# Kernel tuning notes

Measured on AMD Instinct MI355X. Metric: run time of the kernel, lower is better.

Reference implementation:

```python
import jax, jax.numpy as jnp
import numpy as np

N = 50000          # nodes
E = 800000         # edges (before self-loops)
F_IN = 256         # feature_dim
HEADS = 3
OUT = 128          # per-head channels
HO = HEADS * OUT   # 384
NUM_GRAPHS = 64
NUM_CLASSES = 2
SLOPE = 0.2        # PyG GATConv default negative_slope


def setup_inputs() -> dict:
    key = jax.random.key(0)
    ks = jax.random.split(key, 8)
    x = jax.random.normal(ks[0], (N, F_IN), dtype=jnp.float32)
    edge_index = jax.random.randint(ks[1], (2, E), 0, N)
    batch = jnp.sort(jax.random.randint(ks[2], (N,), 0, NUM_GRAPHS))
    # GATConv params (glorot-ish scales)
    W = jax.random.normal(ks[3], (F_IN, HO), dtype=jnp.float32) * (1.0 / np.sqrt(F_IN))
    att_src = jax.random.normal(ks[4], (HEADS, OUT), dtype=jnp.float32) * 0.1
    att_dst = jax.random.normal(ks[5], (HEADS, OUT), dtype=jnp.float32) * 0.1
    bias = jnp.zeros((HO,), dtype=jnp.float32)
    fc_w = jax.random.normal(ks[6], (HO, NUM_CLASSES), dtype=jnp.float32) * 0.05
    fc_b = jnp.zeros((NUM_CLASSES,), dtype=jnp.float32)
    return {"x": x, "edge_index": edge_index, "batch": batch, "W": W,
            "att_src": att_src, "att_dst": att_dst, "bias": bias,
            "fc_w": fc_w, "fc_b": fc_b}


def reference(x, edge_index, batch, W, att_src, att_dst, bias, fc_w, fc_b):
    n = x.shape[0]
    h = (x @ W).reshape(n, HEADS, OUT)                      # [N, H, C]
    # add self-loops (PyG default add_self_loops=True)
    loops = jnp.arange(n)
    src = jnp.concatenate([edge_index[0], loops])           # [E+N]
    dst = jnp.concatenate([edge_index[1], loops])
    # per-node attention logits
    a_src = jnp.einsum('nhc,hc->nh', h, att_src)            # [N, H]
    a_dst = jnp.einsum('nhc,hc->nh', h, att_dst)
    e = jax.nn.leaky_relu(a_src[src] + a_dst[dst], SLOPE)   # [E+N, H]
    # segment softmax over incoming edges of each dst node
    emax = jax.ops.segment_max(e, dst, num_segments=n)
    ex = jnp.exp(e - emax[dst])
    denom = jax.ops.segment_sum(ex, dst, num_segments=n)
    alpha = ex / (denom[dst] + 1e-16)                       # [E+N, H]
    # weighted scatter-add aggregation
    msg = h[src] * alpha[:, :, None]                        # [E+N, H, C]
    out = jax.ops.segment_sum(msg, dst, num_segments=n)     # [N, H, C]
    out = jax.nn.relu(out.reshape(n, HO) + bias)            # [N, 384]
    # global mean pool per graph
    counts = jax.ops.segment_sum(jnp.ones((n,), out.dtype), batch,
                                 num_segments=NUM_GRAPHS)
    pooled = jax.ops.segment_sum(out, batch, num_segments=NUM_GRAPHS)
    pooled = pooled / jnp.maximum(counts, 1.0)[:, None]     # [G, 384]
    return pooled @ fc_w + fc_b                             # [G, num_classes]
```

## Files before the change

kernel.cpp:

```cpp
#include <hip/hip_runtime.h>
#include <hip/hip_bf16.h>
#include <math.h>

#define HEADS 3
#define HO 384
#define NGRAPH 64
#define F_IN 256
#define SLOPE 0.2f

typedef __attribute__((ext_vector_type(8))) short bf8;
typedef __attribute__((ext_vector_type(4))) float f4;
typedef __attribute__((ext_vector_type(2))) unsigned u2v;
typedef __attribute__((ext_vector_type(4))) unsigned u4v;

__device__ __forceinline__ unsigned short bfr(float f) {
    unsigned u = __float_as_uint(f);
    u += 0x7fffu + ((u >> 16) & 1u);
    return (unsigned short)(u >> 16);
}
__device__ __forceinline__ float bflo(unsigned u) { return __uint_as_float(u << 16); }
__device__ __forceinline__ float bfhi(unsigned u) { return __uint_as_float(u & 0xffff0000u); }
__device__ __forceinline__ float lrelu(float v) { return (v > 0.f) ? v : SLOPE * v; }

__device__ __forceinline__ void dec_fma(float* acc, float wm, unsigned ux, unsigned uy) {
    acc[0] += wm * (float)((signed char)(ux));
    acc[1] += wm * (float)((signed char)(ux >> 8));
    acc[2] += wm * (float)((signed char)(ux >> 16));
    acc[3] += wm * (float)((signed char)(ux >> 24));
    acc[4] += wm * (float)((signed char)(uy));
    acc[5] += wm * (float)((signed char)(uy >> 8));
    acc[6] += wm * (float)((signed char)(uy >> 16));
    acc[7] += wm * (float)((signed char)(uy >> 24));
}

__global__ __launch_bounds__(256) void misc_k(const int* __restrict__ ei,
                                              const float* __restrict__ W,
                                              const int* __restrict__ batch,
                                              int* __restrict__ count,
                                              int* __restrict__ rank,
                                              short* __restrict__ WbT,
                                              int* __restrict__ gstart,
                                              int NBc, int E, int N) {
    int b = blockIdx.x;
    if (b < NBc) {
        int e = b * 256 + threadIdx.x;
        int ET = E + N;
        if (e >= ET) return;
        int d = (e < E) ? ei[E + e] : (e - E);
        rank[e] = atomicAdd(&count[d], 1);
    } else if (b < NBc + 384) {
        int n = b - NBc;
        int k = threadIdx.x;
        WbT[n * 256 + k] = (short)bfr(W[(size_t)k * HO + n]);
    } else {
        int g = threadIdx.x;
        if (g > NGRAPH) return;
        int lo = 0, hi = N;
        while (lo < hi) { int mid = (lo + hi) >> 1; if (batch[mid] < g) lo = mid + 1; else hi = mid; }
        gstart[g] = lo;
    }
}

#define XS_STRIDE 40
__global__ __launch_bounds__(256, 3) void gemm_att(const float* __restrict__ X,
                                                   const short* __restrict__ WbT,
                                                   const float* __restrict__ att_src,
                                                   const float* __restrict__ att_dst,
                                                   signed char* __restrict__ hc,
                                                   float* __restrict__ ni,
                                                   float* __restrict__ aDstO, int N) {
    __shared__ short Xs[64 * XS_STRIDE];
    __shared__ short Bs[384 * XS_STRIDE];
    __shared__ float lsS[64][8];
    __shared__ float lsD[64][8];
    __shared__ float lsM[64][8];
    __shared__ float sclS[64][4];
    int t = threadIdx.x;
    int w = t >> 6, lane = t & 63;
    int quad = lane >> 4, l15 = lane & 15;
    int rbase = blockIdx.x * 64;

    int sr = t >> 2;
    int sko = (t & 3) * 8;
    int xrow = rbase + sr;
    xrow = (xrow < N) ? xrow : (N - 1);
    const float* xrp = X + (size_t)xrow * F_IN;

    f4 acc[4][6] = {};

    float4 p0 = *(const float4*)(xrp + sko);
    float4 p1 = *(const float4*)(xrp + sko + 4);

    for (int k0 = 0; k0 < F_IN; k0 += 32) {
        __syncthreads();
        {
            bf8 pk;
            pk[0] = (short)bfr(p0.x); pk[1] = (short)bfr(p0.y);
            pk[2] = (short)bfr(p0.z); pk[3] = (short)bfr(p0.w);
            pk[4] = (short)bfr(p1.x); pk[5] = (short)bfr(p1.y);
            pk[6] = (short)bfr(p1.z); pk[7] = (short)bfr(p1.w);
            *(bf8*)(&Xs[sr * XS_STRIDE + sko]) = pk;
        }
#pragma unroll
        for (int i = 0; i < 6; i++) {
            int n = i * 64 + sr;
            bf8 b = *(const bf8*)(WbT + (size_t)n * F_IN + k0 + sko);
            *(bf8*)(&Bs[n * XS_STRIDE + sko]) = b;
        }
        __syncthreads();
        if (k0 + 32 < F_IN) {
            p0 = *(const float4*)(xrp + k0 + 32 + sko);
            p1 = *(const float4*)(xrp + k0 + 32 + sko + 4);
        }
        bf8 ar[4], br[6];
#pragma unroll
        for (int at = 0; at < 4; at++)
            ar[at] = *(const bf8*)(&Xs[(at * 16 + l15) * XS_STRIDE + quad * 8]);
#pragma unroll
        for (int nt = 0; nt < 6; nt++)
            br[nt] = *(const bf8*)(&Bs[(w * 96 + nt * 16 + l15) * XS_STRIDE + quad * 8]);
#pragma unroll
        for (int at = 0; at < 4; at++)
#pragma unroll
            for (int nt = 0; nt < 6; nt++)
                acc[at][nt] = __builtin_amdgcn_mfma_f32_16x16x32_bf16(ar[at], br[nt], acc[at][nt], 0, 0, 0);
    }

    const int splits[4] = {6, 2, 4, 0};
    int split = splits[w];
    float asv[6], adv[6];
#pragma unroll
    for (int nt = 0; nt < 6; nt++) {
        int c = w * 96 + nt * 16 + l15;
        asv[nt] = att_src[c];
        adv[nt] = att_dst[c];
    }
#pragma unroll
    for (int at = 0; at < 4; at++) {
#pragma unroll
        for (int r = 0; r < 4; r++) {
            float paS = 0.f, pbS = 0.f, paD = 0.f, pbD = 0.f;
#pragma unroll
            for (int nt = 0; nt < 6; nt++) {
                float v = acc[at][nt][r];
                if (nt < split) { paS += v * asv[nt]; paD += v * adv[nt]; }
                else            { pbS += v * asv[nt]; pbD += v * adv[nt]; }
            }
#pragma unroll
            for (int off = 1; off < 16; off <<= 1) {
                paS += __shfl_xor(paS, off); pbS += __shfl_xor(pbS, off);
                paD += __shfl_xor(paD, off); pbD += __shfl_xor(pbD, off);
            }
            if (l15 == 0) {
                int row = at * 16 + quad * 4 + r;
                lsS[row][w * 2 + 0] = paS; lsS[row][w * 2 + 1] = pbS;
                lsD[row][w * 2 + 0] = paD; lsD[row][w * 2 + 1] = pbD;
            }
        }
    }
#pragma unroll
    for (int at = 0; at < 4; at++) {
#pragma unroll
        for (int r = 0; r < 4; r++) {
            float pa = 0.f, pb = 0.f;
#pragma unroll
            for (int nt = 0; nt < 6; nt++) {
                float v = fabsf(acc[at][nt][r]);
                if (nt < split) pa = fmaxf(pa, v); else pb = fmaxf(pb, v);
            }
#pragma unroll
            for (int off = 1; off < 16; off <<= 1) {
                pa = fmaxf(pa, __shfl_xor(pa, off));
                pb = fmaxf(pb, __shfl_xor(pb, off));
            }
            if (l15 == 0) {
                int row = at * 16 + quad * 4 + r;
                lsM[row][w * 2 + 0] = pa; lsM[row][w * 2 + 1] = pb;
            }
        }
    }
    __syncthreads();
    if (t < 64) {
        float s0 = fmaxf(lsM[t][0], lsM[t][2]);
        float s1 = fmaxf(lsM[t][3], lsM[t][4]);
        float s2 = fmaxf(lsM[t][5], lsM[t][7]);
        sclS[t][0] = (s0 > 0.f) ? 127.f / s0 : 0.f;
        sclS[t][1] = (s1 > 0.f) ? 127.f / s1 : 0.f;
        sclS[t][2] = (s2 > 0.f) ? 127.f / s2 : 0.f;
        int node = rbase + t;
        if (node < N) {
            aDstO[node * 3 + 0] = lsD[t][0] + lsD[t][2];
            aDstO[node * 3 + 1] = lsD[t][3] + lsD[t][4];
            aDstO[node * 3 + 2] = lsD[t][5] + lsD[t][7];
            float4 nA, nB;
            nA.x = lsS[t][0] + lsS[t][2];
            nA.y = lsS[t][3] + lsS[t][4];
            nA.z = lsS[t][5] + lsS[t][7];
            nA.w = s0 / 127.f;
            nB.x = s1 / 127.f;
            nB.y = s2 / 127.f;
            nB.z = 0.f; nB.w = 0.f;
            *(float4*)(ni + (size_t)node * 8) = nA;
            *(float4*)(ni + (size_t)node * 8 + 4) = nB;
        }
    }
    __syncthreads();
#pragma unroll
    for (int at = 0; at < 4; at++) {
#pragma unroll
        for (int nt = 0; nt < 6; nt++) {
            int hd = (w * 96 + nt * 16) >> 7;
#pragma unroll
            for (int r = 0; r < 4; r++) {
                int row = at * 16 + quad * 4 + r;
                int node = rbase + row;
                float rq = sclS[row][hd];
                int qi = (int)rintf(acc[at][nt][r] * rq);
                if (node < N) hc[(size_t)node * 384 + w * 96 + nt * 16 + l15] = (signed char)qi;
            }
        }
    }
}

__global__ __launch_bounds__(256) void scan_a(const int* __restrict__ count,
                                              int* __restrict__ offsets,
                                              int* __restrict__ bsums, int N) {
    __shared__ int tmp[256];
    int t = threadIdx.x;
    int i = blockIdx.x * 256 + t;
    int v = (i < N) ? count[i] : 0;
    tmp[t] = v;
    __syncthreads();
    for (int off = 1; off < 256; off <<= 1) {
        int x = (t >= off) ? tmp[t - off] : 0;
        __syncthreads();
        tmp[t] += x;
        __syncthreads();
    }
    if (i < N) offsets[i] = tmp[t] - v;
    if (t == 255) bsums[blockIdx.x] = tmp[255];
}

__global__ __launch_bounds__(256) void scan_b(int* __restrict__ bsums, int NB) {
    __shared__ int tmp[256];
    int t = threadIdx.x;
    int v = (t < NB) ? bsums[t] : 0;
    tmp[t] = v;
    __syncthreads();
    for (int off = 1; off < 256; off <<= 1) {
        int x = (t >= off) ? tmp[t - off] : 0;
        __syncthreads();
        tmp[t] += x;
        __syncthreads();
    }
    if (t < NB) bsums[t] = tmp[t] - v;
}

__global__ __launch_bounds__(256) void scan_c(int* __restrict__ offsets,
                                              const int* __restrict__ bsums, int N) {
    int i = blockIdx.x * 256 + threadIdx.x;
    if (i < N) offsets[i] += bsums[blockIdx.x];
}

__global__ __launch_bounds__(256) void scatter_k(const int* __restrict__ ei,
                                                 const int* __restrict__ rank,
                                                 const int* __restrict__ offsets,
                                                 int* __restrict__ csr_src, int E, int N) {
    int e = blockIdx.x * 256 + threadIdx.x;
    int ET = E + N;
    if (e >= ET) return;
    int s, d;
    if (e < E) { s = ei[e]; d = ei[E + e]; } else { s = e - E; d = s; }
    csr_src[offsets[d] + rank[e]] = s;
}

__global__ __launch_bounds__(256) void aggregate_k(const unsigned* __restrict__ hcw,
                                                   const int* __restrict__ csr_src,
                                                   const int* __restrict__ offsets,
                                                   const int* __restrict__ count,
                                                   const float* __restrict__ ni,
                                                   const float* __restrict__ a_dst,
                                                   const float* __restrict__ bias,
                                                   unsigned* __restrict__ outb, int N) {
    int wid = blockIdx.x * 4 + (threadIdx.x >> 6);
    int lane = threadIdx.x & 63;
    if (wid >= N) return;
    int start = offsets[wid], n = count[wid];
    float ad0 = a_dst[wid * 3 + 0], ad1 = a_dst[wid * 3 + 1], ad2 = a_dst[wid * 3 + 2];
    int head_my = lane >> 4;
    int off = (lane < 48) ? 2 * lane : 0;
    float acc[8] = {0.f, 0.f, 0.f, 0.f, 0.f, 0.f, 0.f, 0.f};
    float i0, i1, i2;

    if (n <= 64) {
        int sreg = 0;
        float l0 = -INFINITY, l1 = -INFINITY, l2 = -INFINITY;
        float s0v = 0.f, s1v = 0.f, s2v = 0.f;
        if (lane < n) {
            sreg = csr_src[start + lane];
            float4 A = *(const float4*)(ni + (size_t)sreg * 8);
            float4 B = *(const float4*)(ni + (size_t)sreg * 8 + 4);
            l0 = lrelu(A.x + ad0); l1 = lrelu(A.y + ad1); l2 = lrelu(A.z + ad2);
            s0v = A.w; s1v = B.x; s2v = B.y;
        }
        float m0 = l0, m1 = l1, m2 = l2;
#pragma unroll
        for (int o = 1; o < 64; o <<= 1) {
            m0 = fmaxf(m0, __shfl_xor(m0, o));
            m1 = fmaxf(m1, __shfl_xor(m1, o));
            m2 = fmaxf(m2, __shfl_xor(m2, o));
        }
        float e0 = (lane < n) ? expf(l0 - m0) : 0.f;
        float e1 = (lane < n) ? expf(l1 - m1) : 0.f;
        float e2 = (lane < n) ? expf(l2 - m2) : 0.f;
        float s0 = e0, s1 = e1, s2 = e2;
#pragma unroll
        for (int o = 1; o < 64; o <<= 1) {
            s0 += __shfl_xor(s0, o);
            s1 += __shfl_xor(s1, o);
            s2 += __shfl_xor(s2, o);
        }
        i0 = 1.f / (s0 + 1e-16f); i1 = 1.f / (s1 + 1e-16f); i2 = 1.f / (s2 + 1e-16f);
        float f0 = e0 * s0v, f1 = e1 * s1v, f2 = e2 * s2v;

        for (int j = 0; j < n; j += 8) {
            unsigned ux[8], uy[8];
#pragma unroll
            for (int q = 0; q < 8; q++) {
                int s = __shfl(sreg, j + q);
                u2v u = *(const u2v*)(hcw + (size_t)s * 96 + off);
                ux[q] = u.x; uy[q] = u.y;
            }
#pragma unroll
            for (int q = 0; q < 8; q++) {
                float w0 = __shfl(f0, j + q);
                float w1 = __shfl(f1, j + q);
                float w2 = __shfl(f2, j + q);
                float wm = (head_my == 0) ? w0 : ((head_my == 1) ? w1 : w2);
                dec_fma(acc, wm, ux[q], uy[q]);
            }
        }
    } else {
        float m0 = -INFINITY, m1 = -INFINITY, m2 = -INFINITY;
        for (int j = lane; j < n; j += 64) {
            int s = csr_src[start + j];
            float4 A = *(const float4*)(ni + (size_t)s * 8);
            m0 = fmaxf(m0, lrelu(A.x + ad0));
            m1 = fmaxf(m1, lrelu(A.y + ad1));
            m2 = fmaxf(m2, lrelu(A.z + ad2));
        }
#pragma unroll
        for (int o = 1; o < 64; o <<= 1) {
            m0 = fmaxf(m0, __shfl_xor(m0, o));
            m1 = fmaxf(m1, __shfl_xor(m1, o));
            m2 = fmaxf(m2, __shfl_xor(m2, o));
        }
        float s0 = 0.f, s1 = 0.f, s2 = 0.f;
        for (int j = lane; j < n; j += 64) {
            int s = csr_src[start + j];
            float4 A = *(const float4*)(ni + (size_t)s * 8);
            s0 += expf(lrelu(A.x + ad0) - m0);
            s1 += expf(lrelu(A.y + ad1) - m1);
            s2 += expf(lrelu(A.z + ad2) - m2);
        }
#pragma unroll
        for (int o = 1; o < 64; o <<= 1) {
            s0 += __shfl_xor(s0, o);
            s1 += __shfl_xor(s1, o);
            s2 += __shfl_xor(s2, o);
        }
        i0 = 1.f / (s0 + 1e-16f); i1 = 1.f / (s1 + 1e-16f); i2 = 1.f / (s2 + 1e-16f);
        for (int j = 0; j < n; j++) {
            int s = csr_src[start + j];
            float4 A = *(const float4*)(ni + (size_t)s * 8);
            float4 B = *(const float4*)(ni + (size_t)s * 8 + 4);
            float w0 = expf(lrelu(A.x + ad0) - m0) * A.w;
            float w1 = expf(lrelu(A.y + ad1) - m1) * B.x;
            float w2 = expf(lrelu(A.z + ad2) - m2) * B.y;
            float wm = (head_my == 0) ? w0 : ((head_my == 1) ? w1 : w2);
            u2v u = *(const u2v*)(hcw + (size_t)s * 96 + off);
            dec_fma(acc, wm, u.x, u.y);
        }
    }

    if (lane < 48) {
        float im = ((head_my == 0) ? i0 : (head_my == 1) ? i1 : i2);
        float4 b0 = *(const float4*)(bias + 8 * lane);
        float4 b1 = *(const float4*)(bias + 8 * lane + 4);
        float bb[8] = {b0.x, b0.y, b0.z, b0.w, b1.x, b1.y, b1.z, b1.w};
        u4v pk;
#pragma unroll
        for (int j = 0; j < 4; j++) {
            float x0 = acc[2 * j] * im + bb[2 * j];
            float x1 = acc[2 * j + 1] * im + bb[2 * j + 1];
            x0 = (x0 > 0.f) ? x0 : 0.f;
            x1 = (x1 > 0.f) ? x1 : 0.f;
            pk[j] = (unsigned)bfr(x0) | ((unsigned)bfr(x1) << 16);
        }
        *(u4v*)(outb + (size_t)wid * 192 + 4 * lane) = pk;
    }
}

__global__ __launch_bounds__(192) void pool_k(const unsigned* __restrict__ outb,
                                              const int* __restrict__ gstart,
                                              float* __restrict__ pooled) {
    int g = blockIdx.x;
    int chunk = blockIdx.y;
    int t = threadIdx.x;
    int lo = gstart[g], hi = gstart[g + 1];
    float al = 0.f, ah = 0.f;
    for (int r = lo + chunk; r < hi; r += 8) {
        unsigned u = outb[(size_t)r * 192 + t];
        al += bflo(u);
        ah += bfhi(u);
    }
    atomicAdd(&pooled[g * HO + 2 * t], al);
    atomicAdd(&pooled[g * HO + 2 * t + 1], ah);
}

__global__ __launch_bounds__(64) void fc_k(const float* __restrict__ pooled,
                                           const int* __restrict__ gstart,
                                           const float* __restrict__ fc_w,
                                           const float* __restrict__ fc_b,
                                           float* __restrict__ out) {
    int g = blockIdx.x;
    int lane = threadIdx.x;
    float a0 = 0.f, a1 = 0.f;
#pragma unroll
    for (int k = 0; k < 6; k++) {
        int c = lane + 64 * k;
        float pv = pooled[g * HO + c];
        a0 += pv * fc_w[c * 2 + 0];
        a1 += pv * fc_w[c * 2 + 1];
    }
#pragma unroll
    for (int off = 32; off > 0; off >>= 1) {
        a0 += __shfl_down(a0, off);
        a1 += __shfl_down(a1, off);
    }
    if (lane == 0) {
        float cnt = fmaxf((float)(gstart[g + 1] - gstart[g]), 1.0f);
        out[g * 2 + 0] = a0 / cnt + fc_b[0];
        out[g * 2 + 1] = a1 / cnt + fc_b[1];
    }
}

extern "C" void kernel_launch(void* const* d_in, const int* in_sizes, int n_in,
                              void* d_out, int out_size, void* d_ws, size_t ws_size,
                              hipStream_t stream) {
    const float* x       = (const float*)d_in[0];
    const int*   ei      = (const int*)d_in[1];
    const int*   batch   = (const int*)d_in[2];
    const float* W       = (const float*)d_in[3];
    const float* att_src = (const float*)d_in[4];
    const float* att_dst = (const float*)d_in[5];
    const float* bias    = (const float*)d_in[6];
    const float* fc_w    = (const float*)d_in[7];
    const float* fc_b    = (const float*)d_in[8];
    float* out = (float*)d_out;

    const int N = in_sizes[2];
    const int E = in_sizes[1] / 2;
    const int ET = E + N;

    char* p = (char*)d_ws;
    auto alloc = [&](size_t bytes) -> char* {
        char* r = p;
        p += (bytes + 255) & ~(size_t)255;
        return r;
    };
    short*       wbt    = (short*)alloc((size_t)HO * F_IN * 2);
    signed char* hc     = (signed char*)alloc((size_t)N * 384);
    unsigned*    outb   = (unsigned*)alloc((size_t)N * 192 * 4);
    float*       ni     = (float*)alloc((size_t)N * 8 * 4);
    float*       a_dst  = (float*)alloc((size_t)N * 3 * 4);
    char*        zstart = p;
    int*         count  = (int*)alloc((size_t)N * 4);
    float*       pooled = (float*)alloc((size_t)NGRAPH * HO * 4);
    size_t       zbytes = (size_t)(p - zstart);
    int*         offsets = (int*)alloc((size_t)N * 4);
    int*         rank    = (int*)alloc((size_t)ET * 4);
    int*         bsums   = (int*)alloc(4096);
    int*         gstart  = (int*)alloc(1024);
    int*         csr_src = (int*)alloc((size_t)ET * 4);

    hipMemsetAsync(zstart, 0, zbytes, stream);

    int NBc = (ET + 255) / 256;
    misc_k<<<NBc + 384 + 1, 256, 0, stream>>>(ei, W, batch, count, rank, wbt, gstart,
                                              NBc, E, N);
    gemm_att<<<(N + 63) / 64, 256, 0, stream>>>(x, wbt, att_src, att_dst,
                                                hc, ni, a_dst, N);
    int NB = (N + 255) / 256;
    scan_a<<<NB, 256, 0, stream>>>(count, offsets, bsums, N);
    scan_b<<<1, 256, 0, stream>>>(bsums, NB);
    scan_c<<<NB, 256, 0, stream>>>(offsets, bsums, N);
    scatter_k<<<(ET + 255) / 256, 256, 0, stream>>>(ei, rank, offsets, csr_src, E, N);
    aggregate_k<<<(N + 3) / 4, 256, 0, stream>>>((const unsigned*)hc, csr_src, offsets,
                                                 count, ni, a_dst, bias, outb, N);
    dim3 pg(NGRAPH, 8);
    pool_k<<<pg, 192, 0, stream>>>(outb, gstart, pooled);
    fc_k<<<NGRAPH, 64, 0, stream>>>(pooled, gstart, fc_w, fc_b, out);

    (void)n_in; (void)out_size; (void)ws_size;
}
```

Measured before the change: 312.7 us.

## Decode int8 features via fp16 magic-number perm and v_fma_mix in aggregation

The gemm now stores quantized features as unsigned bytes with a +128 offset. In aggregation, each byte pair is packed with 0x64 into fp16 values (1024+128+q) using v_perm, and accumulated with v_fma_mix_f32. The constant offset is removed at the end by subtracting 1152 times the summed weights. Per-edge weights and source indices are staged in shared memory, replacing per-edge shuffles. This cuts ALU work for the int8 decode and shuffle, at the cost of larger accumulator magnitudes, which may lose some fp32 precision.

```diff
diff --git a/kernel.cpp b/kernel.cpp
--- a/kernel.cpp
+++ b/kernel.cpp
@@ -22,15 +22,22 @@
 __device__ __forceinline__ float bfhi(unsigned u) { return __uint_as_float(u & 0xffff0000u); }
 __device__ __forceinline__ float lrelu(float v) { return (v > 0.f) ? v : SLOPE * v; }
 
-__device__ __forceinline__ void dec_fma(float* acc, float wm, unsigned ux, unsigned uy) {
-    acc[0] += wm * (float)((signed char)(ux));
-    acc[1] += wm * (float)((signed char)(ux >> 8));
-    acc[2] += wm * (float)((signed char)(ux >> 16));
-    acc[3] += wm * (float)((signed char)(ux >> 24));
-    acc[4] += wm * (float)((signed char)(uy));
-    acc[5] += wm * (float)((signed char)(uy >> 8));
-    acc[6] += wm * (float)((signed char)(uy >> 16));
-    acc[7] += wm * (float)((signed char)(uy >> 24));
+__device__ __forceinline__ void mix2(float& a0, float& a1, unsigned h2, float wm) {
+    asm("v_fma_mix_f32 %0, %2, %3, %0 op_sel:[0,0,0] op_sel_hi:[1,0,0]\n\t"
+        "v_fma_mix_f32 %1, %2, %3, %1 op_sel:[1,0,0] op_sel_hi:[1,0,0]"
+        : "+v"(a0), "+v"(a1)
+        : "v"(h2), "v"(wm));
+}
+__device__ __forceinline__ void dec8_mix(float* acc, float wm, unsigned ux, unsigned uy,
+                                         unsigned c64) {
+    unsigned p0 = __builtin_amdgcn_perm(ux, c64, 0x00050004u);
+    unsigned p1 = __builtin_amdgcn_perm(ux, c64, 0x00070006u);
+    unsigned p2 = __builtin_amdgcn_perm(uy, c64, 0x00050004u);
+    unsigned p3 = __builtin_amdgcn_perm(uy, c64, 0x00070006u);
+    mix2(acc[0], acc[1], p0, wm);
+    mix2(acc[2], acc[3], p1, wm);
+    mix2(acc[4], acc[5], p2, wm);
+    mix2(acc[6], acc[7], p3, wm);
 }
 
 __global__ __launch_bounds__(256) void misc_k(const int* __restrict__ ei,
@@ -66,7 +73,7 @@
                                                    const short* __restrict__ WbT,
                                                    const float* __restrict__ att_src,
                                                    const float* __restrict__ att_dst,
-                                                   signed char* __restrict__ hc,
+                                                   unsigned char* __restrict__ hc,
                                                    float* __restrict__ ni,
                                                    float* __restrict__ aDstO, int N) {
     __shared__ short Xs[64 * XS_STRIDE];
@@ -215,8 +222,8 @@
                 int row = at * 16 + quad * 4 + r;
                 int node = rbase + row;
                 float rq = sclS[row][hd];
-                int qi = (int)rintf(acc[at][nt][r] * rq);
-                if (node < N) hc[(size_t)node * 384 + w * 96 + nt * 16 + l15] = (signed char)qi;
+                int qi = (int)rintf(acc[at][nt][r] * rq) + 128;
+                if (node < N) hc[(size_t)node * 384 + w * 96 + nt * 16 + l15] = (unsigned char)qi;
             }
         }
     }
@@ -282,15 +289,20 @@
                                                    const float* __restrict__ a_dst,
                                                    const float* __restrict__ bias,
                                                    unsigned* __restrict__ outb, int N) {
-    int wid = blockIdx.x * 4 + (threadIdx.x >> 6);
+    __shared__ float ws[4][3][68];
+    __shared__ int   si[4][64];
+    int wv = threadIdx.x >> 6;
+    int wid = blockIdx.x * 4 + wv;
     int lane = threadIdx.x & 63;
     if (wid >= N) return;
     int start = offsets[wid], n = count[wid];
     float ad0 = a_dst[wid * 3 + 0], ad1 = a_dst[wid * 3 + 1], ad2 = a_dst[wid * 3 + 2];
-    int head_my = lane >> 4;
+    int hm = (lane < 48) ? (lane >> 4) : 0;
     int off = (lane < 48) ? 2 * lane : 0;
     float acc[8] = {0.f, 0.f, 0.f, 0.f, 0.f, 0.f, 0.f, 0.f};
+    float wsum = 0.f;
     float i0, i1, i2;
+    const unsigned c64 = 0x64646464u;
 
     if (n <= 64) {
         int sreg = 0;
@@ -321,24 +333,34 @@
             s2 += __shfl_xor(s2, o);
         }
         i0 = 1.f / (s0 + 1e-16f); i1 = 1.f / (s1 + 1e-16f); i2 = 1.f / (s2 + 1e-16f);
-        float f0 = e0 * s0v, f1 = e1 * s1v, f2 = e2 * s2v;
+        ws[wv][0][lane] = e0 * s0v;
+        ws[wv][1][lane] = e1 * s1v;
+        ws[wv][2][lane] = e2 * s2v;
+        si[wv][lane] = sreg;
+        __builtin_amdgcn_wave_barrier();
 
         for (int j = 0; j < n; j += 8) {
-            unsigned ux[8], uy[8];
-#pragma unroll
-            for (int q = 0; q < 8; q++) {
-                int s = __shfl(sreg, j + q);
-                u2v u = *(const u2v*)(hcw + (size_t)s * 96 + off);
-                ux[q] = u.x; uy[q] = u.y;
-            }
-#pragma unroll
-            for (int q = 0; q < 8; q++) {
-                float w0 = __shfl(f0, j + q);
-                float w1 = __shfl(f1, j + q);
-                float w2 = __shfl(f2, j + q);
-                float wm = (head_my == 0) ? w0 : ((head_my == 1) ? w1 : w2);
-                dec_fma(acc, wm, ux[q], uy[q]);
-            }
+            int4 ia = *(const int4*)&si[wv][j];
+            int4 ib = *(const int4*)&si[wv][j + 4];
+            u2v u0 = *(const u2v*)(hcw + (size_t)ia.x * 96 + off);
+            u2v u1 = *(const u2v*)(hcw + (size_t)ia.y * 96 + off);
+            u2v u2 = *(const u2v*)(hcw + (size_t)ia.z * 96 + off);
+            u2v u3 = *(const u2v*)(hcw + (size_t)ia.w * 96 + off);
+            u2v u4 = *(const u2v*)(hcw + (size_t)ib.x * 96 + off);
+            u2v u5 = *(const u2v*)(hcw + (size_t)ib.y * 96 + off);
+            u2v u6 = *(const u2v*)(hcw + (size_t)ib.z * 96 + off);
+            u2v u7 = *(const u2v*)(hcw + (size_t)ib.w * 96 + off);
+            float4 wa = *(const float4*)&ws[wv][hm][j];
+            float4 wb = *(const float4*)&ws[wv][hm][j + 4];
+            wsum += (wa.x + wa.y + wa.z + wa.w) + (wb.x + wb.y + wb.z + wb.w);
+            dec8_mix(acc, wa.x, u0.x, u0.y, c64);
+            dec8_mix(acc, wa.y, u1.x, u1.y, c64);
+            dec8_mix(acc, wa.z, u2.x, u2.y, c64);
+            dec8_mix(acc, wa.w, u3.x, u3.y, c64);
+            dec8_mix(acc, wb.x, u4.x, u4.y, c64);
+            dec8_mix(acc, wb.y, u5.x, u5.y, c64);
+            dec8_mix(acc, wb.z, u6.x, u6.y, c64);
+            dec8_mix(acc, wb.w, u7.x, u7.y, c64);
         }
     } else {
         float m0 = -INFINITY, m1 = -INFINITY, m2 = -INFINITY;
@@ -377,22 +399,24 @@
             float w0 = expf(lrelu(A.x + ad0) - m0) * A.w;
             float w1 = expf(lrelu(A.y + ad1) - m1) * B.x;
             float w2 = expf(lrelu(A.z + ad2) - m2) * B.y;
-            float wm = (head_my == 0) ? w0 : ((head_my == 1) ? w1 : w2);
+            float wm = (hm == 0) ? w0 : ((hm == 1) ? w1 : w2);
             u2v u = *(const u2v*)(hcw + (size_t)s * 96 + off);
-            dec_fma(acc, wm, u.x, u.y);
+            wsum += wm;
+            dec8_mix(acc, wm, u.x, u.y, c64);
         }
     }
 
     if (lane < 48) {
-        float im = ((head_my == 0) ? i0 : (head_my == 1) ? i1 : i2);
+        float im = (hm == 0) ? i0 : ((hm == 1) ? i1 : i2);
+        float corr = 1152.f * wsum;
         float4 b0 = *(const float4*)(bias + 8 * lane);
         float4 b1 = *(const float4*)(bias + 8 * lane + 4);
         float bb[8] = {b0.x, b0.y, b0.z, b0.w, b1.x, b1.y, b1.z, b1.w};
         u4v pk;
 #pragma unroll
         for (int j = 0; j < 4; j++) {
-            float x0 = acc[2 * j] * im + bb[2 * j];
-            float x1 = acc[2 * j + 1] * im + bb[2 * j + 1];
+            float x0 = (acc[2 * j] - corr) * im + bb[2 * j];
+            float x1 = (acc[2 * j + 1] - corr) * im + bb[2 * j + 1];
             x0 = (x0 > 0.f) ? x0 : 0.f;
             x1 = (x1 > 0.f) ? x1 : 0.f;
             pk[j] = (unsigned)bfr(x0) | ((unsigned)bfr(x1) << 16);
@@ -469,20 +493,20 @@
         p += (bytes + 255) & ~(size_t)255;
         return r;
     };
-    short*       wbt    = (short*)alloc((size_t)HO * F_IN * 2);
-    signed char* hc     = (signed char*)alloc((size_t)N * 384);
-    unsigned*    outb   = (unsigned*)alloc((size_t)N * 192 * 4);
-    float*       ni     = (float*)alloc((size_t)N * 8 * 4);
-    float*       a_dst  = (float*)alloc((size_t)N * 3 * 4);
-    char*        zstart = p;
-    int*         count  = (int*)alloc((size_t)N * 4);
-    float*       pooled = (float*)alloc((size_t)NGRAPH * HO * 4);
-    size_t       zbytes = (size_t)(p - zstart);
-    int*         offsets = (int*)alloc((size_t)N * 4);
-    int*         rank    = (int*)alloc((size_t)ET * 4);
-    int*         bsums   = (int*)alloc(4096);
-    int*         gstart  = (int*)alloc(1024);
-    int*         csr_src = (int*)alloc((size_t)ET * 4);
+    short*         wbt    = (short*)alloc((size_t)HO * F_IN * 2);
+    unsigned char* hc     = (unsigned char*)alloc((size_t)N * 384);
+    unsigned*      outb   = (unsigned*)alloc((size_t)N * 192 * 4);
+    float*         ni     = (float*)alloc((size_t)N * 8 * 4);
+    float*         a_dst  = (float*)alloc((size_t)N * 3 * 4);
+    char*          zstart = p;
+    int*           count  = (int*)alloc((size_t)N * 4);
+    float*         pooled = (float*)alloc((size_t)NGRAPH * HO * 4);
+    size_t         zbytes = (size_t)(p - zstart);
+    int*           offsets = (int*)alloc((size_t)N * 4);
+    int*           rank    = (int*)alloc((size_t)ET * 4);
+    int*           bsums   = (int*)alloc(4096);
+    int*           gstart  = (int*)alloc(1024);
+    int*           csr_src = (int*)alloc((size_t)ET * 4);
 
     hipMemsetAsync(zstart, 0, zbytes, stream);
 
```

Result: faster. 298.2 us (-4.6%).
